# Kernel optimization log

Measured on AMD Instinct MI355X. Metric: run time of the kernel, lower is better.

Reference implementation:

```python
import jax, jax.numpy as jnp
import numpy as np

N, E = 50000, 800000
IN_F, HID, OUT, HEADS = 128, 64, 128, 4
NEG_SLOPE = 0.2


def setup_inputs() -> dict:
    key = jax.random.key(0)
    ks = jax.random.split(key, 10)
    s = 0.05
    return {
        "x": jax.random.normal(ks[0], (N, IN_F), dtype=jnp.float32),
        "edge_index": jax.random.randint(ks[1], (2, E), 0, N, dtype=jnp.int64),
        "W1": jax.random.normal(ks[2], (IN_F, HEADS * HID), dtype=jnp.float32) * s,
        "att_src1": jax.random.normal(ks[3], (HEADS, HID), dtype=jnp.float32) * s,
        "att_dst1": jax.random.normal(ks[4], (HEADS, HID), dtype=jnp.float32) * s,
        "b1": jnp.zeros((HEADS * HID,), dtype=jnp.float32),
        "W2": jax.random.normal(ks[5], (HEADS * HID, OUT), dtype=jnp.float32) * s,
        "att_src2": jax.random.normal(ks[6], (1, OUT), dtype=jnp.float32) * s,
        "att_dst2": jax.random.normal(ks[7], (1, OUT), dtype=jnp.float32) * s,
        "b2": jnp.zeros((OUT,), dtype=jnp.float32),
    }


def _gat_layer(x, W, a_src, a_dst, b, src, dst, heads, out_c):
    n = x.shape[0]
    h = (x @ W).reshape(n, heads, out_c)              # [N, H, C]
    alpha_s = jnp.einsum("nhc,hc->nh", h, a_src)       # [N, H]
    alpha_d = jnp.einsum("nhc,hc->nh", h, a_dst)
    e = jax.nn.leaky_relu(alpha_s[src] + alpha_d[dst], NEG_SLOPE)  # [E, H]
    # scatter-softmax over edges grouped by destination node
    m = jax.ops.segment_max(e, dst, num_segments=n)
    ex = jnp.exp(e - m[dst])
    denom = jax.ops.segment_sum(ex, dst, num_segments=n)
    alpha = ex / denom[dst]                            # [E, H]
    out = jax.ops.segment_sum(alpha[:, :, None] * h[src], dst, num_segments=n)
    return out.reshape(n, heads * out_c) + b


def reference(x, edge_index, W1, att_src1, att_dst1, b1, W2, att_src2, att_dst2, b2):
    n = x.shape[0]
    loop = jnp.arange(n, dtype=edge_index.dtype)       # PyG add_self_loops=True
    src = jnp.concatenate([edge_index[0], loop])
    dst = jnp.concatenate([edge_index[1], loop])
    h = _gat_layer(x, W1, att_src1, att_dst1, b1, src, dst, HEADS, HID)
    h = jax.nn.elu(h)
    out = _gat_layer(h, W2, att_src2, att_dst2, b2, src, dst, 1, OUT)
    return out
```

## Files before the change

kernel.cpp:

```cpp
#include <hip/hip_runtime.h>
#include <hip/hip_bf16.h>

#define NEG_SLOPE 0.2f

typedef short bf16x8 __attribute__((ext_vector_type(8)));
typedef float f32x4 __attribute__((ext_vector_type(4)));
typedef float f32x2 __attribute__((ext_vector_type(2)));

__device__ __forceinline__ unsigned short f2bf(float f) {
    unsigned int x = __float_as_uint(f);
    unsigned int lsb = (x >> 16) & 1u;
    x += 0x7fffu + lsb;
    return (unsigned short)(x >> 16);
}
__device__ __forceinline__ f32x2 upk(unsigned int u) {
    f32x2 r;
    r.x = __uint_as_float(u << 16);
    r.y = __uint_as_float(u & 0xffff0000u);
    return r;
}
__device__ __forceinline__ unsigned short f2h(float f) {
    _Float16 h = (_Float16)f;
    return *(unsigned short*)&h;
}
__device__ __forceinline__ float h2f(unsigned short u) {
    _Float16 h = *(_Float16*)&u;
    return (float)h;
}

__device__ __forceinline__ int bsum_excl(const int* __restrict__ bsum, int nb, int blk) {
    int lane = threadIdx.x & 63;
    int v = (lane < nb) ? bsum[lane] : 0;
    int x = v;
    #pragma unroll
    for (int off = 1; off < 64; off <<= 1) {
        int t = __shfl_up(x, off);
        if (lane >= off) x += t;
    }
    return __shfl(x - v, blk);
}

__global__ void prep_kernel(const float* __restrict__ W1, const float* __restrict__ W2,
                            unsigned short* __restrict__ wt1, unsigned short* __restrict__ wt2,
                            int* __restrict__ deg, int N) {
    int idx = blockIdx.x * 256 + threadIdx.x;
    if (idx < 128 * 256) {
        int k = idx >> 8, n = idx & 255;
        wt1[(size_t)n * 128 + k] = f2bf(W1[idx]);
    } else if (idx < 2 * 128 * 256) {
        int j = idx - 128 * 256;
        int k = j >> 7, n = j & 127;
        wt2[(size_t)n * 256 + k] = f2bf(W2[j]);
    } else {
        int i = idx - 2 * 128 * 256;
        if (i < N) deg[i] = 0;
    }
}

__global__ void degree_kernel(const int* __restrict__ ei, int E, int N,
                              int* __restrict__ deg, int* __restrict__ idx) {
    int e = blockIdx.x * blockDim.x + threadIdx.x;
    int EA = E + N;
    if (e >= EA) return;
    int dst = (e < E) ? ei[E + e] : (e - E);
    idx[e] = atomicAdd(&deg[dst], 1);
}

__global__ void scan_local(const int* __restrict__ deg, int* __restrict__ offs,
                           int* __restrict__ bsum, int N) {
    __shared__ int wsum[16];
    int tid = threadIdx.x;
    int lane = tid & 63;
    int wave = tid >> 6;
    int i = blockIdx.x * 1024 + tid;
    int v = (i < N) ? deg[i] : 0;
    int x = v;
    #pragma unroll
    for (int off = 1; off < 64; off <<= 1) {
        int t = __shfl_up(x, off);
        if (lane >= off) x += t;
    }
    if (lane == 63) wsum[wave] = x;
    __syncthreads();
    if (wave == 0 && lane < 16) {
        int w = wsum[lane];
        #pragma unroll
        for (int off = 1; off < 16; off <<= 1) {
            int t = __shfl_up(w, off);
            if (lane >= off) w += t;
        }
        wsum[lane] = w;
    }
    __syncthreads();
    int wexcl = (wave > 0) ? wsum[wave - 1] : 0;
    if (i <= N) offs[i] = wexcl + x - v;
    if (tid == 0) bsum[blockIdx.x] = wsum[15];
}

__global__ void scatter_kernel(const int* __restrict__ ei, int E, int N,
                               const int* __restrict__ offs, const int* __restrict__ idx,
                               const int* __restrict__ bsum, int nb,
                               const float* __restrict__ as1, const float* __restrict__ ad1,
                               int* __restrict__ colb, uint2* __restrict__ p1) {
    int e = blockIdx.x * blockDim.x + threadIdx.x;
    int EA = E + N;
    bool act = e < EA;
    int s = 0, d = 0;
    if (act) {
        if (e < E) { s = ei[e]; d = ei[E + e]; }
        else       { s = d = e - E; }
    }
    int excl = bsum_excl(bsum, nb, d >> 10);
    if (!act) return;
    int pos = offs[d] + excl + idx[e];
    colb[pos] = s << 9;
    float4 av = *(const float4*)(as1 + s * 4);
    float4 dv = *(const float4*)(ad1 + d * 4);
    float e0 = av.x + dv.x, e1 = av.y + dv.y, e2 = av.z + dv.z, e3 = av.w + dv.w;
    e0 = (e0 > 0.f) ? e0 : NEG_SLOPE * e0;
    e1 = (e1 > 0.f) ? e1 : NEG_SLOPE * e1;
    e2 = (e2 > 0.f) ? e2 : NEG_SLOPE * e2;
    e3 = (e3 > 0.f) ? e3 : NEG_SLOPE * e3;
    uint2 q;
    q.x = (unsigned int)f2h(__expf(e0)) | ((unsigned int)f2h(__expf(e1)) << 16);
    q.y = (unsigned int)f2h(__expf(e2)) | ((unsigned int)f2h(__expf(e3)) << 16);
    p1[pos] = q;
}

__global__ void gemm1_mfma(const float* __restrict__ A,
                           const unsigned short* __restrict__ Wt,
                           const float* __restrict__ att_s, const float* __restrict__ att_d,
                           unsigned short* __restrict__ hb,
                           float* __restrict__ as, float* __restrict__ ad, int M) {
    int wave = threadIdx.x >> 6;
    int lane = threadIdx.x & 63;
    int quad = lane >> 4;
    int l16 = lane & 15;
    int m0 = blockIdx.x * 64 + wave * 16;
    int rowc = min(m0 + l16, M - 1);
    bf16x8 a[4];
    const float* ap = A + (size_t)rowc * 128 + quad * 8;
    #pragma unroll
    for (int kc = 0; kc < 4; ++kc) {
        float4 f0 = *(const float4*)(ap + kc * 32);
        float4 f1 = *(const float4*)(ap + kc * 32 + 4);
        bf16x8 v;
        v[0] = (short)f2bf(f0.x); v[1] = (short)f2bf(f0.y);
        v[2] = (short)f2bf(f0.z); v[3] = (short)f2bf(f0.w);
        v[4] = (short)f2bf(f1.x); v[5] = (short)f2bf(f1.y);
        v[6] = (short)f2bf(f1.z); v[7] = (short)f2bf(f1.w);
        a[kc] = v;
    }
    f32x4 acc[16];
    #pragma unroll
    for (int nt = 0; nt < 16; ++nt) {
        f32x4 c = {0.f, 0.f, 0.f, 0.f};
        const unsigned short* bp = Wt + (size_t)(nt * 16 + l16) * 128 + quad * 8;
        #pragma unroll
        for (int kc = 0; kc < 4; ++kc) {
            bf16x8 b = *(const bf16x8*)(bp + kc * 32);
            c = __builtin_amdgcn_mfma_f32_16x16x32_bf16(a[kc], b, c, 0, 0, 0);
        }
        acc[nt] = c;
    }
    float asv[16], adv[16];
    #pragma unroll
    for (int nt = 0; nt < 16; ++nt) {
        asv[nt] = att_s[nt * 16 + l16];
        adv[nt] = att_d[nt * 16 + l16];
    }
    int srow0 = m0 + quad * 4;
    #pragma unroll
    for (int r = 0; r < 4; ++r) {
        int srow = srow0 + r;
        bool ok = srow < M;
        if (ok) {
            #pragma unroll
            for (int nt = 0; nt < 16; ++nt)
                hb[(size_t)srow * 256 + nt * 16 + l16] = f2bf(acc[nt][r]);
        }
        #pragma unroll
        for (int h = 0; h < 4; ++h) {
            float ps = acc[4 * h][r] * asv[4 * h] + acc[4 * h + 1][r] * asv[4 * h + 1]
                     + acc[4 * h + 2][r] * asv[4 * h + 2] + acc[4 * h + 3][r] * asv[4 * h + 3];
            float pd = acc[4 * h][r] * adv[4 * h] + acc[4 * h + 1][r] * adv[4 * h + 1]
                     + acc[4 * h + 2][r] * adv[4 * h + 2] + acc[4 * h + 3][r] * adv[4 * h + 3];
            #pragma unroll
            for (int off = 1; off < 16; off <<= 1) {
                ps += __shfl_xor(ps, off);
                pd += __shfl_xor(pd, off);
            }
            if (ok && l16 == 0) {
                as[srow * 4 + h] = ps;
                ad[srow * 4 + h] = pd;
            }
        }
    }
}

__global__ void gemm2_mfma(const unsigned short* __restrict__ Ab,
                           const unsigned short* __restrict__ Wt,
                           const float* __restrict__ att_s, const float* __restrict__ att_d,
                           unsigned short* __restrict__ hb,
                           float* __restrict__ as, float* __restrict__ ad, int M) {
    int wave = threadIdx.x >> 6;
    int lane = threadIdx.x & 63;
    int quad = lane >> 4;
    int l16 = lane & 15;
    int m0 = blockIdx.x * 64 + wave * 16;
    int rowc = min(m0 + l16, M - 1);
    bf16x8 a[8];
    const unsigned short* ap = Ab + (size_t)rowc * 256 + quad * 8;
    #pragma unroll
    for (int kc = 0; kc < 8; ++kc) a[kc] = *(const bf16x8*)(ap + kc * 32);
    f32x4 acc[8];
    #pragma unroll
    for (int nt = 0; nt < 8; ++nt) {
        f32x4 c = {0.f, 0.f, 0.f, 0.f};
        const unsigned short* bp = Wt + (size_t)(nt * 16 + l16) * 256 + quad * 8;
        #pragma unroll
        for (int kc = 0; kc < 8; ++kc) {
            bf16x8 b = *(const bf16x8*)(bp + kc * 32);
            c = __builtin_amdgcn_mfma_f32_16x16x32_bf16(a[kc], b, c, 0, 0, 0);
        }
        acc[nt] = c;
    }
    float asv[8], adv[8];
    #pragma unroll
    for (int nt = 0; nt < 8; ++nt) {
        asv[nt] = att_s[nt * 16 + l16];
        adv[nt] = att_d[nt * 16 + l16];
    }
    int srow0 = m0 + quad * 4;
    #pragma unroll
    for (int r = 0; r < 4; ++r) {
        int srow = srow0 + r;
        bool ok = srow < M;
        if (ok) {
            #pragma unroll
            for (int nt = 0; nt < 8; ++nt)
                hb[(size_t)srow * 128 + nt * 16 + l16] = f2bf(acc[nt][r]);
        }
        float ps = 0.f, pd = 0.f;
        #pragma unroll
        for (int nt = 0; nt < 8; ++nt) {
            ps = fmaf(acc[nt][r], asv[nt], ps);
            pd = fmaf(acc[nt][r], adv[nt], pd);
        }
        #pragma unroll
        for (int off = 1; off < 16; off <<= 1) {
            ps += __shfl_xor(ps, off);
            pd += __shfl_xor(pd, off);
        }
        if (ok && l16 == 0) { as[srow] = ps; ad[srow] = pd; }
    }
}

__global__ void agg1_kernel(const unsigned short* __restrict__ hb,
                            const int* __restrict__ colb, const uint2* __restrict__ p1,
                            const int* __restrict__ offs,
                            const int* __restrict__ bsum, int nb,
                            const float* __restrict__ b1,
                            unsigned short* __restrict__ out, int N) {
    int node = blockIdx.x * 4 + (threadIdx.x >> 6);
    if (node >= N) return;
    int lane = threadIdx.x & 63;
    int half = lane >> 5;
    int sub  = lane & 31;
    int head = sub >> 3;
    int c0b = sub * 16;
    const char* hpc = (const char*)hb;
    int beg = offs[node] + bsum_excl(bsum, nb, node >> 10);
    int end = offs[node + 1] + bsum_excl(bsum, nb, (node + 1) >> 10);
    float d = 0.f;
    f32x2 acc[4] = {};
    int j = beg + half;
    for (; j + 6 < end; j += 8) {
        int o0 = colb[j] + c0b;
        int o1 = colb[j + 2] + c0b;
        int o2 = colb[j + 4] + c0b;
        int o3 = colb[j + 6] + c0b;
        uint2 q0 = p1[j];
        uint2 q1 = p1[j + 2];
        uint2 q2 = p1[j + 4];
        uint2 q3 = p1[j + 6];
        uint4 g0 = *(const uint4*)(hpc + o0);
        uint4 g1 = *(const uint4*)(hpc + o1);
        uint4 g2 = *(const uint4*)(hpc + o2);
        uint4 g3 = *(const uint4*)(hpc + o3);
        unsigned int u0 = (head & 2) ? q0.y : q0.x;
        unsigned int u1 = (head & 2) ? q1.y : q1.x;
        unsigned int u2 = (head & 2) ? q2.y : q2.x;
        unsigned int u3 = (head & 2) ? q3.y : q3.x;
        float p0 = h2f((unsigned short)((head & 1) ? (u0 >> 16) : (u0 & 0xffff)));
        float p1v = h2f((unsigned short)((head & 1) ? (u1 >> 16) : (u1 & 0xffff)));
        float p2 = h2f((unsigned short)((head & 1) ? (u2 >> 16) : (u2 & 0xffff)));
        float p3 = h2f((unsigned short)((head & 1) ? (u3 >> 16) : (u3 & 0xffff)));
        d += (p0 + p1v) + (p2 + p3);
        const unsigned int* w0 = (const unsigned int*)&g0;
        const unsigned int* w1 = (const unsigned int*)&g1;
        const unsigned int* w2 = (const unsigned int*)&g2;
        const unsigned int* w3 = (const unsigned int*)&g3;
        f32x2 v0 = {p0, p0}, v1 = {p1v, p1v}, v2 = {p2, p2}, v3 = {p3, p3};
        #pragma unroll
        for (int i = 0; i < 4; ++i) {
            acc[i] = __builtin_elementwise_fma(v0, upk(w0[i]), acc[i]);
            acc[i] = __builtin_elementwise_fma(v1, upk(w1[i]), acc[i]);
            acc[i] = __builtin_elementwise_fma(v2, upk(w2[i]), acc[i]);
            acc[i] = __builtin_elementwise_fma(v3, upk(w3[i]), acc[i]);
        }
    }
    for (; j < end; j += 2) {
        int o = colb[j] + c0b;
        uint2 q = p1[j];
        uint4 g = *(const uint4*)(hpc + o);
        unsigned int u = (head & 2) ? q.y : q.x;
        float p = h2f((unsigned short)((head & 1) ? (u >> 16) : (u & 0xffff)));
        d += p;
        const unsigned int* w = (const unsigned int*)&g;
        f32x2 v = {p, p};
        #pragma unroll
        for (int i = 0; i < 4; ++i)
            acc[i] = __builtin_elementwise_fma(v, upk(w[i]), acc[i]);
    }
    d += __shfl_xor(d, 32);
    #pragma unroll
    for (int i = 0; i < 4; ++i) {
        acc[i].x += __shfl_xor(acc[i].x, 32);
        acc[i].y += __shfl_xor(acc[i].y, 32);
    }
    if (half == 0) {
        float inv = 1.f / d;
        int c0 = sub * 8;
        float4 bb0 = *(const float4*)(b1 + c0);
        float4 bb1 = *(const float4*)(b1 + c0 + 4);
        float av[8] = {acc[0].x, acc[0].y, acc[1].x, acc[1].y,
                       acc[2].x, acc[2].y, acc[3].x, acc[3].y};
        float bb[8] = {bb0.x, bb0.y, bb0.z, bb0.w, bb1.x, bb1.y, bb1.z, bb1.w};
        unsigned short o[8];
        #pragma unroll
        for (int i = 0; i < 8; ++i) {
            float v = av[i] * inv + bb[i];
            v = (v > 0.f) ? v : (__expf(v) - 1.f);
            o[i] = f2bf(v);
        }
        ushort4 q0 = {o[0], o[1], o[2], o[3]};
        ushort4 q1 = {o[4], o[5], o[6], o[7]};
        *(ushort4*)(out + (size_t)node * 256 + c0) = q0;
        *(ushort4*)(out + (size_t)node * 256 + c0 + 4) = q1;
    }
}

__global__ void agg2_kernel(const unsigned short* __restrict__ hb,
                            const float* __restrict__ as,
                            const float* __restrict__ ad,
                            const int* __restrict__ offs, const int* __restrict__ colb,
                            const int* __restrict__ bsum, int nb,
                            const float* __restrict__ b2,
                            float* __restrict__ out, int N) {
    int node = blockIdx.x * 4 + (threadIdx.x >> 6);
    if (node >= N) return;
    int lane = threadIdx.x & 63;
    int q   = lane >> 4;
    int sub = lane & 15;
    int c0b = sub * 16;
    const char* hpc = (const char*)hb;
    float adv = ad[node];
    int beg = offs[node] + bsum_excl(bsum, nb, node >> 10);
    int end = offs[node + 1] + bsum_excl(bsum, nb, (node + 1) >> 10);
    float d = 0.f;
    f32x2 acc[4] = {};
    int j = beg + q;
    for (; j + 4 < end; j += 8) {
        int cb0 = colb[j];
        int cb1 = colb[j + 4];
        uint4 g0 = *(const uint4*)(hpc + (cb0 >> 1) + c0b);
        uint4 g1 = *(const uint4*)(hpc + (cb1 >> 1) + c0b);
        float e0 = as[cb0 >> 9] + adv;
        float e1 = as[cb1 >> 9] + adv;
        e0 = (e0 > 0.f) ? e0 : NEG_SLOPE * e0;
        e1 = (e1 > 0.f) ? e1 : NEG_SLOPE * e1;
        float p0 = __expf(e0), p1 = __expf(e1);
        d += p0 + p1;
        const unsigned int* w0 = (const unsigned int*)&g0;
        const unsigned int* w1 = (const unsigned int*)&g1;
        f32x2 v0 = {p0, p0}, v1 = {p1, p1};
        #pragma unroll
        for (int i = 0; i < 4; ++i) {
            acc[i] = __builtin_elementwise_fma(v0, upk(w0[i]), acc[i]);
            acc[i] = __builtin_elementwise_fma(v1, upk(w1[i]), acc[i]);
        }
    }
    for (; j < end; j += 4) {
        int cb = colb[j];
        uint4 g = *(const uint4*)(hpc + (cb >> 1) + c0b);
        float e = as[cb >> 9] + adv;
        e = (e > 0.f) ? e : NEG_SLOPE * e;
        float p = __expf(e);
        d += p;
        const unsigned int* w = (const unsigned int*)&g;
        f32x2 v = {p, p};
        #pragma unroll
        for (int i = 0; i < 4; ++i)
            acc[i] = __builtin_elementwise_fma(v, upk(w[i]), acc[i]);
    }
    d += __shfl_xor(d, 16);
    d += __shfl_xor(d, 32);
    #pragma unroll
    for (int i = 0; i < 4; ++i) {
        acc[i].x += __shfl_xor(acc[i].x, 16);
        acc[i].x += __shfl_xor(acc[i].x, 32);
        acc[i].y += __shfl_xor(acc[i].y, 16);
        acc[i].y += __shfl_xor(acc[i].y, 32);
    }
    if (lane < 16) {
        float inv = 1.f / d;
        int c0 = sub * 8;
        float4 bb0 = *(const float4*)(b2 + c0);
        float4 bb1 = *(const float4*)(b2 + c0 + 4);
        float av[8] = {acc[0].x, acc[0].y, acc[1].x, acc[1].y,
                       acc[2].x, acc[2].y, acc[3].x, acc[3].y};
        float bb[8] = {bb0.x, bb0.y, bb0.z, bb0.w, bb1.x, bb1.y, bb1.z, bb1.w};
        *(float4*)(out + (size_t)node * 128 + c0) =
            make_float4(av[0] * inv + bb[0], av[1] * inv + bb[1],
                        av[2] * inv + bb[2], av[3] * inv + bb[3]);
        *(float4*)(out + (size_t)node * 128 + c0 + 4) =
            make_float4(av[4] * inv + bb[4], av[5] * inv + bb[5],
                        av[6] * inv + bb[6], av[7] * inv + bb[7]);
    }
}


extern "C" void kernel_launch(void* const* d_in, const int* in_sizes, int n_in,
                              void* d_out, int out_size, void* d_ws, size_t ws_size,
                              hipStream_t stream) {
    const float* x    = (const float*)d_in[0];
    const int*   ei   = (const int*)d_in[1];
    const float* W1   = (const float*)d_in[2];
    const float* at_s1 = (const float*)d_in[3];
    const float* at_d1 = (const float*)d_in[4];
    const float* b1   = (const float*)d_in[5];
    const float* W2   = (const float*)d_in[6];
    const float* at_s2 = (const float*)d_in[7];
    const float* at_d2 = (const float*)d_in[8];
    const float* b2   = (const float*)d_in[9];
    float* out = (float*)d_out;

    const int N  = in_sizes[0] / 128;
    const int E  = in_sizes[1] / 2;
    const int EA = E + N;

    char* ws = (char*)d_ws;
    size_t off = 0;
    auto alloc = [&](size_t bytes) -> void* {
        void* p = ws + off;
        off += (bytes + 255) & ~(size_t)255;
        return p;
    };
    unsigned short* wt1  = (unsigned short*)alloc((size_t)256 * 128 * 2);
    unsigned short* wt2  = (unsigned short*)alloc((size_t)128 * 256 * 2);
    unsigned short* h1b  = (unsigned short*)alloc((size_t)N * 256 * 2);
    unsigned short* h1ab = (unsigned short*)alloc((size_t)N * 256 * 2);
    unsigned short* h2b  = (unsigned short*)alloc((size_t)N * 128 * 2);
    float* as1 = (float*)alloc((size_t)N * 4 * 4);
    float* ad1 = (float*)alloc((size_t)N * 4 * 4);
    float* as2 = (float*)alloc((size_t)N * 4);
    float* ad2 = (float*)alloc((size_t)N * 4);
    int* deg  = (int*)alloc((size_t)N * 4);
    int* idx  = (int*)alloc((size_t)EA * 4);
    int* offs = (int*)alloc((size_t)(N + 1) * 4);
    int* bsum = (int*)alloc((size_t)1024 * 4);
    int* colb = (int*)alloc((size_t)EA * 4);
    uint2* p1 = (uint2*)alloc((size_t)EA * 8);

    const int nb = (N + 1 + 1023) / 1024;

    prep_kernel<<<(2 * 128 * 256 + N + 255) / 256, 256, 0, stream>>>(W1, W2, wt1, wt2, deg, N);
    degree_kernel<<<(EA + 255) / 256, 256, 0, stream>>>(ei, E, N, deg, idx);
    scan_local<<<nb, 1024, 0, stream>>>(deg, offs, bsum, N);

    gemm1_mfma<<<(N + 63) / 64, 256, 0, stream>>>(x, wt1, at_s1, at_d1, h1b, as1, ad1, N);
    scatter_kernel<<<(EA + 255) / 256, 256, 0, stream>>>(ei, E, N, offs, idx, bsum, nb,
                                                         as1, ad1, colb, p1);
    agg1_kernel<<<(N + 3) / 4, 256, 0, stream>>>(h1b, colb, p1, offs, bsum, nb, b1, h1ab, N);

    gemm2_mfma<<<(N + 63) / 64, 256, 0, stream>>>(h1ab, wt2, at_s2, at_d2, h2b, as2, ad2, N);
    agg2_kernel<<<(N + 3) / 4, 256, 0, stream>>>(h2b, as2, ad2, offs, colb, bsum, nb,
                                                 b2, out, N);
}
```

Measured before the change: 332.9 us.

## Fuse layer-1 aggregation with layer-2 GEMM through shared-memory tile

Merges agg1 and gemm2 into one kernel. Each block aggregates 16 nodes (4 per wave) into an LDS bf16 tile, then runs MFMA against W2, with each wave covering 2 of the 8 output column tiles and combining the attention dot products via LDS atomics. This removes the global write and re-read of the N×256 intermediate and one kernel launch. In exchange each wave now processes 4 nodes one after another, the block has a barrier before the GEMM, and every block reloads W2 from cache.

```diff
diff --git a/kernel.cpp b/kernel.cpp
--- a/kernel.cpp
+++ b/kernel.cpp
@@ -198,156 +198,158 @@
     }
 }
 
-__global__ void gemm2_mfma(const unsigned short* __restrict__ Ab,
+__global__ void agg1_gemm2(const unsigned short* __restrict__ hb,
+                           const int* __restrict__ colb, const uint2* __restrict__ p1,
+                           const int* __restrict__ offs,
+                           const int* __restrict__ bsum, int nb,
+                           const float* __restrict__ b1,
                            const unsigned short* __restrict__ Wt,
                            const float* __restrict__ att_s, const float* __restrict__ att_d,
-                           unsigned short* __restrict__ hb,
-                           float* __restrict__ as, float* __restrict__ ad, int M) {
-    int wave = threadIdx.x >> 6;
-    int lane = threadIdx.x & 63;
-    int quad = lane >> 4;
-    int l16 = lane & 15;
-    int m0 = blockIdx.x * 64 + wave * 16;
-    int rowc = min(m0 + l16, M - 1);
-    bf16x8 a[8];
-    const unsigned short* ap = Ab + (size_t)rowc * 256 + quad * 8;
-    #pragma unroll
-    for (int kc = 0; kc < 8; ++kc) a[kc] = *(const bf16x8*)(ap + kc * 32);
-    f32x4 acc[8];
-    #pragma unroll
-    for (int nt = 0; nt < 8; ++nt) {
-        f32x4 c = {0.f, 0.f, 0.f, 0.f};
-        const unsigned short* bp = Wt + (size_t)(nt * 16 + l16) * 256 + quad * 8;
-        #pragma unroll
-        for (int kc = 0; kc < 8; ++kc) {
-            bf16x8 b = *(const bf16x8*)(bp + kc * 32);
-            c = __builtin_amdgcn_mfma_f32_16x16x32_bf16(a[kc], b, c, 0, 0, 0);
-        }
-        acc[nt] = c;
-    }
-    float asv[8], adv[8];
-    #pragma unroll
-    for (int nt = 0; nt < 8; ++nt) {
-        asv[nt] = att_s[nt * 16 + l16];
-        adv[nt] = att_d[nt * 16 + l16];
-    }
-    int srow0 = m0 + quad * 4;
-    #pragma unroll
-    for (int r = 0; r < 4; ++r) {
-        int srow = srow0 + r;
-        bool ok = srow < M;
-        if (ok) {
-            #pragma unroll
-            for (int nt = 0; nt < 8; ++nt)
-                hb[(size_t)srow * 128 + nt * 16 + l16] = f2bf(acc[nt][r]);
-        }
-        float ps = 0.f, pd = 0.f;
-        #pragma unroll
-        for (int nt = 0; nt < 8; ++nt) {
-            ps = fmaf(acc[nt][r], asv[nt], ps);
-            pd = fmaf(acc[nt][r], adv[nt], pd);
-        }
-        #pragma unroll
-        for (int off = 1; off < 16; off <<= 1) {
-            ps += __shfl_xor(ps, off);
-            pd += __shfl_xor(pd, off);
-        }
-        if (ok && l16 == 0) { as[srow] = ps; ad[srow] = pd; }
-    }
-}
-
-__global__ void agg1_kernel(const unsigned short* __restrict__ hb,
-                            const int* __restrict__ colb, const uint2* __restrict__ p1,
-                            const int* __restrict__ offs,
-                            const int* __restrict__ bsum, int nb,
-                            const float* __restrict__ b1,
-                            unsigned short* __restrict__ out, int N) {
-    int node = blockIdx.x * 4 + (threadIdx.x >> 6);
-    if (node >= N) return;
-    int lane = threadIdx.x & 63;
+                           unsigned short* __restrict__ h2b,
+                           float* __restrict__ as2, float* __restrict__ ad2, int N) {
+    __shared__ unsigned short Atile[16][264];
+    __shared__ float asP[16], adP[16];
+    int tid = threadIdx.x;
+    int wave = tid >> 6;
+    int lane = tid & 63;
+    if (tid < 16) { asP[tid] = 0.f; adP[tid] = 0.f; }
     int half = lane >> 5;
     int sub  = lane & 31;
     int head = sub >> 3;
     int c0b = sub * 16;
     const char* hpc = (const char*)hb;
-    int beg = offs[node] + bsum_excl(bsum, nb, node >> 10);
-    int end = offs[node + 1] + bsum_excl(bsum, nb, (node + 1) >> 10);
-    float d = 0.f;
-    f32x2 acc[4] = {};
-    int j = beg + half;
-    for (; j + 6 < end; j += 8) {
-        int o0 = colb[j] + c0b;
-        int o1 = colb[j + 2] + c0b;
-        int o2 = colb[j + 4] + c0b;
-        int o3 = colb[j + 6] + c0b;
-        uint2 q0 = p1[j];
-        uint2 q1 = p1[j + 2];
-        uint2 q2 = p1[j + 4];
-        uint2 q3 = p1[j + 6];
-        uint4 g0 = *(const uint4*)(hpc + o0);
-        uint4 g1 = *(const uint4*)(hpc + o1);
-        uint4 g2 = *(const uint4*)(hpc + o2);
-        uint4 g3 = *(const uint4*)(hpc + o3);
-        unsigned int u0 = (head & 2) ? q0.y : q0.x;
-        unsigned int u1 = (head & 2) ? q1.y : q1.x;
-        unsigned int u2 = (head & 2) ? q2.y : q2.x;
-        unsigned int u3 = (head & 2) ? q3.y : q3.x;
-        float p0 = h2f((unsigned short)((head & 1) ? (u0 >> 16) : (u0 & 0xffff)));
-        float p1v = h2f((unsigned short)((head & 1) ? (u1 >> 16) : (u1 & 0xffff)));
-        float p2 = h2f((unsigned short)((head & 1) ? (u2 >> 16) : (u2 & 0xffff)));
-        float p3 = h2f((unsigned short)((head & 1) ? (u3 >> 16) : (u3 & 0xffff)));
-        d += (p0 + p1v) + (p2 + p3);
-        const unsigned int* w0 = (const unsigned int*)&g0;
-        const unsigned int* w1 = (const unsigned int*)&g1;
-        const unsigned int* w2 = (const unsigned int*)&g2;
-        const unsigned int* w3 = (const unsigned int*)&g3;
-        f32x2 v0 = {p0, p0}, v1 = {p1v, p1v}, v2 = {p2, p2}, v3 = {p3, p3};
+    int node0 = blockIdx.x * 16;
+
+    for (int t = 0; t < 4; ++t) {
+        int lrow = wave * 4 + t;
+        int node = min(node0 + lrow, N - 1);
+        int beg = offs[node] + bsum_excl(bsum, nb, node >> 10);
+        int end = offs[node + 1] + bsum_excl(bsum, nb, (node + 1) >> 10);
+        float d = 0.f;
+        f32x2 acc[4] = {};
+        int j = beg + half;
+        for (; j + 6 < end; j += 8) {
+            int o0 = colb[j] + c0b;
+            int o1 = colb[j + 2] + c0b;
+            int o2 = colb[j + 4] + c0b;
+            int o3 = colb[j + 6] + c0b;
+            uint2 q0 = p1[j];
+            uint2 q1 = p1[j + 2];
+            uint2 q2 = p1[j + 4];
+            uint2 q3 = p1[j + 6];
+            uint4 g0 = *(const uint4*)(hpc + o0);
+            uint4 g1 = *(const uint4*)(hpc + o1);
+            uint4 g2 = *(const uint4*)(hpc + o2);
+            uint4 g3 = *(const uint4*)(hpc + o3);
+            unsigned int u0 = (head & 2) ? q0.y : q0.x;
+            unsigned int u1 = (head & 2) ? q1.y : q1.x;
+            unsigned int u2 = (head & 2) ? q2.y : q2.x;
+            unsigned int u3 = (head & 2) ? q3.y : q3.x;
+            float p0 = h2f((unsigned short)((head & 1) ? (u0 >> 16) : (u0 & 0xffff)));
+            float p1v = h2f((unsigned short)((head & 1) ? (u1 >> 16) : (u1 & 0xffff)));
+            float p2 = h2f((unsigned short)((head & 1) ? (u2 >> 16) : (u2 & 0xffff)));
+            float p3 = h2f((unsigned short)((head & 1) ? (u3 >> 16) : (u3 & 0xffff)));
+            d += (p0 + p1v) + (p2 + p3);
+            const unsigned int* w0 = (const unsigned int*)&g0;
+            const unsigned int* w1 = (const unsigned int*)&g1;
+            const unsigned int* w2 = (const unsigned int*)&g2;
+            const unsigned int* w3 = (const unsigned int*)&g3;
+            f32x2 v0 = {p0, p0}, v1 = {p1v, p1v}, v2 = {p2, p2}, v3 = {p3, p3};
+            #pragma unroll
+            for (int i = 0; i < 4; ++i) {
+                acc[i] = __builtin_elementwise_fma(v0, upk(w0[i]), acc[i]);
+                acc[i] = __builtin_elementwise_fma(v1, upk(w1[i]), acc[i]);
+                acc[i] = __builtin_elementwise_fma(v2, upk(w2[i]), acc[i]);
+                acc[i] = __builtin_elementwise_fma(v3, upk(w3[i]), acc[i]);
+            }
+        }
+        for (; j < end; j += 2) {
+            int o = colb[j] + c0b;
+            uint2 q = p1[j];
+            uint4 g = *(const uint4*)(hpc + o);
+            unsigned int u = (head & 2) ? q.y : q.x;
+            float p = h2f((unsigned short)((head & 1) ? (u >> 16) : (u & 0xffff)));
+            d += p;
+            const unsigned int* w = (const unsigned int*)&g;
+            f32x2 v = {p, p};
+            #pragma unroll
+            for (int i = 0; i < 4; ++i)
+                acc[i] = __builtin_elementwise_fma(v, upk(w[i]), acc[i]);
+        }
+        d += __shfl_xor(d, 32);
         #pragma unroll
         for (int i = 0; i < 4; ++i) {
-            acc[i] = __builtin_elementwise_fma(v0, upk(w0[i]), acc[i]);
-            acc[i] = __builtin_elementwise_fma(v1, upk(w1[i]), acc[i]);
-            acc[i] = __builtin_elementwise_fma(v2, upk(w2[i]), acc[i]);
-            acc[i] = __builtin_elementwise_fma(v3, upk(w3[i]), acc[i]);
-        }
-    }
-    for (; j < end; j += 2) {
-        int o = colb[j] + c0b;
-        uint2 q = p1[j];
-        uint4 g = *(const uint4*)(hpc + o);
-        unsigned int u = (head & 2) ? q.y : q.x;
-        float p = h2f((unsigned short)((head & 1) ? (u >> 16) : (u & 0xffff)));
-        d += p;
-        const unsigned int* w = (const unsigned int*)&g;
-        f32x2 v = {p, p};
-        #pragma unroll
-        for (int i = 0; i < 4; ++i)
-            acc[i] = __builtin_elementwise_fma(v, upk(w[i]), acc[i]);
-    }
-    d += __shfl_xor(d, 32);
-    #pragma unroll
-    for (int i = 0; i < 4; ++i) {
-        acc[i].x += __shfl_xor(acc[i].x, 32);
-        acc[i].y += __shfl_xor(acc[i].y, 32);
-    }
-    if (half == 0) {
-        float inv = 1.f / d;
-        int c0 = sub * 8;
-        float4 bb0 = *(const float4*)(b1 + c0);
-        float4 bb1 = *(const float4*)(b1 + c0 + 4);
-        float av[8] = {acc[0].x, acc[0].y, acc[1].x, acc[1].y,
-                       acc[2].x, acc[2].y, acc[3].x, acc[3].y};
-        float bb[8] = {bb0.x, bb0.y, bb0.z, bb0.w, bb1.x, bb1.y, bb1.z, bb1.w};
-        unsigned short o[8];
-        #pragma unroll
-        for (int i = 0; i < 8; ++i) {
-            float v = av[i] * inv + bb[i];
-            v = (v > 0.f) ? v : (__expf(v) - 1.f);
-            o[i] = f2bf(v);
-        }
-        ushort4 q0 = {o[0], o[1], o[2], o[3]};
-        ushort4 q1 = {o[4], o[5], o[6], o[7]};
-        *(ushort4*)(out + (size_t)node * 256 + c0) = q0;
-        *(ushort4*)(out + (size_t)node * 256 + c0 + 4) = q1;
+            acc[i].x += __shfl_xor(acc[i].x, 32);
+            acc[i].y += __shfl_xor(acc[i].y, 32);
+        }
+        if (half == 0) {
+            float inv = 1.f / d;
+            int c0 = sub * 8;
+            float4 bb0 = *(const float4*)(b1 + c0);
+            float4 bb1 = *(const float4*)(b1 + c0 + 4);
+            float av[8] = {acc[0].x, acc[0].y, acc[1].x, acc[1].y,
+                           acc[2].x, acc[2].y, acc[3].x, acc[3].y};
+            float bb[8] = {bb0.x, bb0.y, bb0.z, bb0.w, bb1.x, bb1.y, bb1.z, bb1.w};
+            unsigned short o[8];
+            #pragma unroll
+            for (int i = 0; i < 8; ++i) {
+                float v = av[i] * inv + bb[i];
+                v = (v > 0.f) ? v : (__expf(v) - 1.f);
+                o[i] = f2bf(v);
+            }
+            ushort4 q0 = {o[0], o[1], o[2], o[3]};
+            ushort4 q1 = {o[4], o[5], o[6], o[7]};
+            *(ushort4*)&Atile[lrow][c0] = q0;
+            *(ushort4*)&Atile[lrow][c0 + 4] = q1;
+        }
+    }
+    __syncthreads();
+
+    int quad = lane >> 4;
+    int l16 = lane & 15;
+    bf16x8 a[8];
+    #pragma unroll
+    for (int kc = 0; kc < 8; ++kc)
+        a[kc] = *(const bf16x8*)&Atile[l16][kc * 32 + quad * 8];
+    int nt0 = wave * 2;
+    f32x4 acc2[2];
+    #pragma unroll
+    for (int i = 0; i < 2; ++i) {
+        f32x4 c = {0.f, 0.f, 0.f, 0.f};
+        const unsigned short* bp = Wt + (size_t)((nt0 + i) * 16 + l16) * 256 + quad * 8;
+        #pragma unroll
+        for (int kc = 0; kc < 8; ++kc) {
+            bf16x8 b = *(const bf16x8*)(bp + kc * 32);
+            c = __builtin_amdgcn_mfma_f32_16x16x32_bf16(a[kc], b, c, 0, 0, 0);
+        }
+        acc2[i] = c;
+    }
+    float s0 = att_s[nt0 * 16 + l16], s1 = att_s[(nt0 + 1) * 16 + l16];
+    float d0 = att_d[nt0 * 16 + l16], d1 = att_d[(nt0 + 1) * 16 + l16];
+    #pragma unroll
+    for (int r = 0; r < 4; ++r) {
+        int row = quad * 4 + r;
+        int grow = node0 + row;
+        if (grow < N) {
+            h2b[(size_t)grow * 128 + nt0 * 16 + l16] = f2bf(acc2[0][r]);
+            h2b[(size_t)grow * 128 + (nt0 + 1) * 16 + l16] = f2bf(acc2[1][r]);
+        }
+        float ps = acc2[0][r] * s0 + acc2[1][r] * s1;
+        float pd = acc2[0][r] * d0 + acc2[1][r] * d1;
+        #pragma unroll
+        for (int off = 1; off < 16; off <<= 1) {
+            ps += __shfl_xor(ps, off);
+            pd += __shfl_xor(pd, off);
+        }
+        if (l16 == 0) {
+            atomicAdd(&asP[row], ps);
+            atomicAdd(&adP[row], pd);
+        }
+    }
+    __syncthreads();
+    if (tid < 16 && node0 + tid < N) {
+        as2[node0 + tid] = asP[tid];
+        ad2[node0 + tid] = adP[tid];
     }
 }
 
@@ -460,7 +462,6 @@
     unsigned short* wt1  = (unsigned short*)alloc((size_t)256 * 128 * 2);
     unsigned short* wt2  = (unsigned short*)alloc((size_t)128 * 256 * 2);
     unsigned short* h1b  = (unsigned short*)alloc((size_t)N * 256 * 2);
-    unsigned short* h1ab = (unsigned short*)alloc((size_t)N * 256 * 2);
     unsigned short* h2b  = (unsigned short*)alloc((size_t)N * 128 * 2);
     float* as1 = (float*)alloc((size_t)N * 4 * 4);
     float* ad1 = (float*)alloc((size_t)N * 4 * 4);
@@ -482,9 +483,8 @@
     gemm1_mfma<<<(N + 63) / 64, 256, 0, stream>>>(x, wt1, at_s1, at_d1, h1b, as1, ad1, N);
     scatter_kernel<<<(EA + 255) / 256, 256, 0, stream>>>(ei, E, N, offs, idx, bsum, nb,
                                                          as1, ad1, colb, p1);
-    agg1_kernel<<<(N + 3) / 4, 256, 0, stream>>>(h1b, colb, p1, offs, bsum, nb, b1, h1ab, N);
-
-    gemm2_mfma<<<(N + 63) / 64, 256, 0, stream>>>(h1ab, wt2, at_s2, at_d2, h2b, as2, ad2, N);
+    agg1_gemm2<<<(N + 15) / 16, 256, 0, stream>>>(h1b, colb, p1, offs, bsum, nb, b1,
+                                                  wt2, at_s2, at_d2, h2b, as2, ad2, N);
     agg2_kernel<<<(N + 3) / 4, 256, 0, stream>>>(h2b, as2, ad2, offs, colb, bsum, nb,
                                                  b2, out, N);
 }
```

Measured after the change: 325.8 us. 2.1% less time.

## Fuse layer-1 aggregation with layer-2 GEMM through an LDS tile

Applied to the files above, without the earlier changes.

Merges the agg1 kernel and gemm2 kernel into one. Each wave aggregates 16 nodes one after another and writes the ELU-activated bf16 rows into an XOR-swizzled shared-memory tile, which then feeds the MFMA GEMM directly. This removes the global write and re-read of the 50000x256 intermediate and one kernel launch. In exchange, each wave handles 16 nodes serially with only 4 waves per block, which lowers the parallelism of the gather phase and may hurt latency hiding. The edge loop may also be unbalanced across the 16 nodes.

```diff
diff --git a/kernel.cpp b/kernel.cpp
--- a/kernel.cpp
+++ b/kernel.cpp
@@ -198,156 +198,160 @@
     }
 }
 
-__global__ void gemm2_mfma(const unsigned short* __restrict__ Ab,
+__global__ void agg1_gemm2(const unsigned short* __restrict__ hb,
+                           const int* __restrict__ colb, const uint2* __restrict__ p1,
+                           const int* __restrict__ offs,
+                           const int* __restrict__ bsum, int nb,
+                           const float* __restrict__ b1,
                            const unsigned short* __restrict__ Wt,
                            const float* __restrict__ att_s, const float* __restrict__ att_d,
-                           unsigned short* __restrict__ hb,
-                           float* __restrict__ as, float* __restrict__ ad, int M) {
-    int wave = threadIdx.x >> 6;
-    int lane = threadIdx.x & 63;
-    int quad = lane >> 4;
-    int l16 = lane & 15;
-    int m0 = blockIdx.x * 64 + wave * 16;
-    int rowc = min(m0 + l16, M - 1);
-    bf16x8 a[8];
-    const unsigned short* ap = Ab + (size_t)rowc * 256 + quad * 8;
-    #pragma unroll
-    for (int kc = 0; kc < 8; ++kc) a[kc] = *(const bf16x8*)(ap + kc * 32);
-    f32x4 acc[8];
-    #pragma unroll
-    for (int nt = 0; nt < 8; ++nt) {
-        f32x4 c = {0.f, 0.f, 0.f, 0.f};
-        const unsigned short* bp = Wt + (size_t)(nt * 16 + l16) * 256 + quad * 8;
-        #pragma unroll
-        for (int kc = 0; kc < 8; ++kc) {
-            bf16x8 b = *(const bf16x8*)(bp + kc * 32);
-            c = __builtin_amdgcn_mfma_f32_16x16x32_bf16(a[kc], b, c, 0, 0, 0);
-        }
-        acc[nt] = c;
-    }
-    float asv[8], adv[8];
-    #pragma unroll
-    for (int nt = 0; nt < 8; ++nt) {
-        asv[nt] = att_s[nt * 16 + l16];
-        adv[nt] = att_d[nt * 16 + l16];
-    }
-    int srow0 = m0 + quad * 4;
-    #pragma unroll
-    for (int r = 0; r < 4; ++r) {
-        int srow = srow0 + r;
-        bool ok = srow < M;
-        if (ok) {
-            #pragma unroll
-            for (int nt = 0; nt < 8; ++nt)
-                hb[(size_t)srow * 128 + nt * 16 + l16] = f2bf(acc[nt][r]);
-        }
-        float ps = 0.f, pd = 0.f;
-        #pragma unroll
-        for (int nt = 0; nt < 8; ++nt) {
-            ps = fmaf(acc[nt][r], asv[nt], ps);
-            pd = fmaf(acc[nt][r], adv[nt], pd);
-        }
-        #pragma unroll
-        for (int off = 1; off < 16; off <<= 1) {
-            ps += __shfl_xor(ps, off);
-            pd += __shfl_xor(pd, off);
-        }
-        if (ok && l16 == 0) { as[srow] = ps; ad[srow] = pd; }
-    }
-}
-
-__global__ void agg1_kernel(const unsigned short* __restrict__ hb,
-                            const int* __restrict__ colb, const uint2* __restrict__ p1,
-                            const int* __restrict__ offs,
-                            const int* __restrict__ bsum, int nb,
-                            const float* __restrict__ b1,
-                            unsigned short* __restrict__ out, int N) {
-    int node = blockIdx.x * 4 + (threadIdx.x >> 6);
-    if (node >= N) return;
-    int lane = threadIdx.x & 63;
+                           unsigned short* __restrict__ h2b,
+                           float* __restrict__ as2, float* __restrict__ ad2, int N) {
+    __shared__ unsigned short tiles[4][16][256];
+    int tid = threadIdx.x;
+    int wave = tid >> 6;
+    int lane = tid & 63;
     int half = lane >> 5;
     int sub  = lane & 31;
     int head = sub >> 3;
     int c0b = sub * 16;
     const char* hpc = (const char*)hb;
-    int beg = offs[node] + bsum_excl(bsum, nb, node >> 10);
-    int end = offs[node + 1] + bsum_excl(bsum, nb, (node + 1) >> 10);
-    float d = 0.f;
-    f32x2 acc[4] = {};
-    int j = beg + half;
-    for (; j + 6 < end; j += 8) {
-        int o0 = colb[j] + c0b;
-        int o1 = colb[j + 2] + c0b;
-        int o2 = colb[j + 4] + c0b;
-        int o3 = colb[j + 6] + c0b;
-        uint2 q0 = p1[j];
-        uint2 q1 = p1[j + 2];
-        uint2 q2 = p1[j + 4];
-        uint2 q3 = p1[j + 6];
-        uint4 g0 = *(const uint4*)(hpc + o0);
-        uint4 g1 = *(const uint4*)(hpc + o1);
-        uint4 g2 = *(const uint4*)(hpc + o2);
-        uint4 g3 = *(const uint4*)(hpc + o3);
-        unsigned int u0 = (head & 2) ? q0.y : q0.x;
-        unsigned int u1 = (head & 2) ? q1.y : q1.x;
-        unsigned int u2 = (head & 2) ? q2.y : q2.x;
-        unsigned int u3 = (head & 2) ? q3.y : q3.x;
-        float p0 = h2f((unsigned short)((head & 1) ? (u0 >> 16) : (u0 & 0xffff)));
-        float p1v = h2f((unsigned short)((head & 1) ? (u1 >> 16) : (u1 & 0xffff)));
-        float p2 = h2f((unsigned short)((head & 1) ? (u2 >> 16) : (u2 & 0xffff)));
-        float p3 = h2f((unsigned short)((head & 1) ? (u3 >> 16) : (u3 & 0xffff)));
-        d += (p0 + p1v) + (p2 + p3);
-        const unsigned int* w0 = (const unsigned int*)&g0;
-        const unsigned int* w1 = (const unsigned int*)&g1;
-        const unsigned int* w2 = (const unsigned int*)&g2;
-        const unsigned int* w3 = (const unsigned int*)&g3;
-        f32x2 v0 = {p0, p0}, v1 = {p1v, p1v}, v2 = {p2, p2}, v3 = {p3, p3};
+    int node0 = blockIdx.x * 64 + wave * 16;
+    unsigned short (*tile)[256] = tiles[wave];
+
+    for (int t = 0; t < 16; ++t) {
+        int node = min(node0 + t, N - 1);
+        int beg = offs[node] + bsum_excl(bsum, nb, node >> 10);
+        int end = offs[node + 1] + bsum_excl(bsum, nb, (node + 1) >> 10);
+        float d = 0.f;
+        f32x2 acc[4] = {};
+        int j = beg + half;
+        for (; j + 6 < end; j += 8) {
+            int o0 = colb[j] + c0b;
+            int o1 = colb[j + 2] + c0b;
+            int o2 = colb[j + 4] + c0b;
+            int o3 = colb[j + 6] + c0b;
+            uint2 q0 = p1[j];
+            uint2 q1 = p1[j + 2];
+            uint2 q2 = p1[j + 4];
+            uint2 q3 = p1[j + 6];
+            uint4 g0 = *(const uint4*)(hpc + o0);
+            uint4 g1 = *(const uint4*)(hpc + o1);
+            uint4 g2 = *(const uint4*)(hpc + o2);
+            uint4 g3 = *(const uint4*)(hpc + o3);
+            unsigned int u0 = (head & 2) ? q0.y : q0.x;
+            unsigned int u1 = (head & 2) ? q1.y : q1.x;
+            unsigned int u2 = (head & 2) ? q2.y : q2.x;
+            unsigned int u3 = (head & 2) ? q3.y : q3.x;
+            float p0 = h2f((unsigned short)((head & 1) ? (u0 >> 16) : (u0 & 0xffff)));
+            float p1v = h2f((unsigned short)((head & 1) ? (u1 >> 16) : (u1 & 0xffff)));
+            float p2 = h2f((unsigned short)((head & 1) ? (u2 >> 16) : (u2 & 0xffff)));
+            float p3 = h2f((unsigned short)((head & 1) ? (u3 >> 16) : (u3 & 0xffff)));
+            d += (p0 + p1v) + (p2 + p3);
+            const unsigned int* w0 = (const unsigned int*)&g0;
+            const unsigned int* w1 = (const unsigned int*)&g1;
+            const unsigned int* w2 = (const unsigned int*)&g2;
+            const unsigned int* w3 = (const unsigned int*)&g3;
+            f32x2 v0 = {p0, p0}, v1 = {p1v, p1v}, v2 = {p2, p2}, v3 = {p3, p3};
+            #pragma unroll
+            for (int i = 0; i < 4; ++i) {
+                acc[i] = __builtin_elementwise_fma(v0, upk(w0[i]), acc[i]);
+                acc[i] = __builtin_elementwise_fma(v1, upk(w1[i]), acc[i]);
+                acc[i] = __builtin_elementwise_fma(v2, upk(w2[i]), acc[i]);
+                acc[i] = __builtin_elementwise_fma(v3, upk(w3[i]), acc[i]);
+            }
+        }
+        for (; j < end; j += 2) {
+            int o = colb[j] + c0b;
+            uint2 q = p1[j];
+            uint4 g = *(const uint4*)(hpc + o);
+            unsigned int u = (head & 2) ? q.y : q.x;
+            float p = h2f((unsigned short)((head & 1) ? (u >> 16) : (u & 0xffff)));
+            d += p;
+            const unsigned int* w = (const unsigned int*)&g;
+            f32x2 v = {p, p};
+            #pragma unroll
+            for (int i = 0; i < 4; ++i)
+                acc[i] = __builtin_elementwise_fma(v, upk(w[i]), acc[i]);
+        }
+        d += __shfl_xor(d, 32);
         #pragma unroll
         for (int i = 0; i < 4; ++i) {
-            acc[i] = __builtin_elementwise_fma(v0, upk(w0[i]), acc[i]);
-            acc[i] = __builtin_elementwise_fma(v1, upk(w1[i]), acc[i]);
-            acc[i] = __builtin_elementwise_fma(v2, upk(w2[i]), acc[i]);
-            acc[i] = __builtin_elementwise_fma(v3, upk(w3[i]), acc[i]);
-        }
-    }
-    for (; j < end; j += 2) {
-        int o = colb[j] + c0b;
-        uint2 q = p1[j];
-        uint4 g = *(const uint4*)(hpc + o);
-        unsigned int u = (head & 2) ? q.y : q.x;
-        float p = h2f((unsigned short)((head & 1) ? (u >> 16) : (u & 0xffff)));
-        d += p;
-        const unsigned int* w = (const unsigned int*)&g;
-        f32x2 v = {p, p};
-        #pragma unroll
-        for (int i = 0; i < 4; ++i)
-            acc[i] = __builtin_elementwise_fma(v, upk(w[i]), acc[i]);
-    }
-    d += __shfl_xor(d, 32);
-    #pragma unroll
-    for (int i = 0; i < 4; ++i) {
-        acc[i].x += __shfl_xor(acc[i].x, 32);
-        acc[i].y += __shfl_xor(acc[i].y, 32);
-    }
-    if (half == 0) {
-        float inv = 1.f / d;
-        int c0 = sub * 8;
-        float4 bb0 = *(const float4*)(b1 + c0);
-        float4 bb1 = *(const float4*)(b1 + c0 + 4);
-        float av[8] = {acc[0].x, acc[0].y, acc[1].x, acc[1].y,
-                       acc[2].x, acc[2].y, acc[3].x, acc[3].y};
-        float bb[8] = {bb0.x, bb0.y, bb0.z, bb0.w, bb1.x, bb1.y, bb1.z, bb1.w};
-        unsigned short o[8];
-        #pragma unroll
-        for (int i = 0; i < 8; ++i) {
-            float v = av[i] * inv + bb[i];
-            v = (v > 0.f) ? v : (__expf(v) - 1.f);
-            o[i] = f2bf(v);
-        }
-        ushort4 q0 = {o[0], o[1], o[2], o[3]};
-        ushort4 q1 = {o[4], o[5], o[6], o[7]};
-        *(ushort4*)(out + (size_t)node * 256 + c0) = q0;
-        *(ushort4*)(out + (size_t)node * 256 + c0 + 4) = q1;
+            acc[i].x += __shfl_xor(acc[i].x, 32);
+            acc[i].y += __shfl_xor(acc[i].y, 32);
+        }
+        if (half == 0) {
+            float inv = 1.f / d;
+            int c0 = sub * 8;
+            float4 bb0 = *(const float4*)(b1 + c0);
+            float4 bb1 = *(const float4*)(b1 + c0 + 4);
+            float av[8] = {acc[0].x, acc[0].y, acc[1].x, acc[1].y,
+                           acc[2].x, acc[2].y, acc[3].x, acc[3].y};
+            float bb[8] = {bb0.x, bb0.y, bb0.z, bb0.w, bb1.x, bb1.y, bb1.z, bb1.w};
+            unsigned short o[8];
+            #pragma unroll
+            for (int i = 0; i < 8; ++i) {
+                float v = av[i] * inv + bb[i];
+                v = (v > 0.f) ? v : (__expf(v) - 1.f);
+                o[i] = f2bf(v);
+            }
+            uint4 pk;
+            pk.x = (unsigned int)o[0] | ((unsigned int)o[1] << 16);
+            pk.y = (unsigned int)o[2] | ((unsigned int)o[3] << 16);
+            pk.z = (unsigned int)o[4] | ((unsigned int)o[5] << 16);
+            pk.w = (unsigned int)o[6] | ((unsigned int)o[7] << 16);
+            *(uint4*)&tile[t][(sub ^ t) * 8] = pk;
+        }
+    }
+
+    int quad = lane >> 4;
+    int l16 = lane & 15;
+    bf16x8 a[8];
+    #pragma unroll
+    for (int kc = 0; kc < 8; ++kc) {
+        int grp = (kc * 4 + quad) ^ l16;
+        a[kc] = *(const bf16x8*)&tile[l16][grp * 8];
+    }
+    f32x4 acc2[8];
+    #pragma unroll
+    for (int nt = 0; nt < 8; ++nt) {
+        f32x4 c = {0.f, 0.f, 0.f, 0.f};
+        const unsigned short* bp = Wt + (size_t)(nt * 16 + l16) * 256 + quad * 8;
+        #pragma unroll
+        for (int kc = 0; kc < 8; ++kc) {
+            bf16x8 b = *(const bf16x8*)(bp + kc * 32);
+            c = __builtin_amdgcn_mfma_f32_16x16x32_bf16(a[kc], b, c, 0, 0, 0);
+        }
+        acc2[nt] = c;
+    }
+    float asv[8], adv[8];
+    #pragma unroll
+    for (int nt = 0; nt < 8; ++nt) {
+        asv[nt] = att_s[nt * 16 + l16];
+        adv[nt] = att_d[nt * 16 + l16];
+    }
+    int srow0 = node0 + quad * 4;
+    #pragma unroll
+    for (int r = 0; r < 4; ++r) {
+        int srow = srow0 + r;
+        bool ok = srow < N;
+        if (ok) {
+            #pragma unroll
+            for (int nt = 0; nt < 8; ++nt)
+                h2b[(size_t)srow * 128 + nt * 16 + l16] = f2bf(acc2[nt][r]);
+        }
+        float ps = 0.f, pd = 0.f;
+        #pragma unroll
+        for (int nt = 0; nt < 8; ++nt) {
+            ps = fmaf(acc2[nt][r], asv[nt], ps);
+            pd = fmaf(acc2[nt][r], adv[nt], pd);
+        }
+        #pragma unroll
+        for (int off = 1; off < 16; off <<= 1) {
+            ps += __shfl_xor(ps, off);
+            pd += __shfl_xor(pd, off);
+        }
+        if (ok && l16 == 0) { as2[srow] = ps; ad2[srow] = pd; }
     }
 }
 
@@ -460,7 +464,6 @@
     unsigned short* wt1  = (unsigned short*)alloc((size_t)256 * 128 * 2);
     unsigned short* wt2  = (unsigned short*)alloc((size_t)128 * 256 * 2);
     unsigned short* h1b  = (unsigned short*)alloc((size_t)N * 256 * 2);
-    unsigned short* h1ab = (unsigned short*)alloc((size_t)N * 256 * 2);
     unsigned short* h2b  = (unsigned short*)alloc((size_t)N * 128 * 2);
     float* as1 = (float*)alloc((size_t)N * 4 * 4);
     float* ad1 = (float*)alloc((size_t)N * 4 * 4);
@@ -482,9 +485,8 @@
     gemm1_mfma<<<(N + 63) / 64, 256, 0, stream>>>(x, wt1, at_s1, at_d1, h1b, as1, ad1, N);
     scatter_kernel<<<(EA + 255) / 256, 256, 0, stream>>>(ei, E, N, offs, idx, bsum, nb,
                                                          as1, ad1, colb, p1);
-    agg1_kernel<<<(N + 3) / 4, 256, 0, stream>>>(h1b, colb, p1, offs, bsum, nb, b1, h1ab, N);
-
-    gemm2_mfma<<<(N + 63) / 64, 256, 0, stream>>>(h1ab, wt2, at_s2, at_d2, h2b, as2, ad2, N);
+    agg1_gemm2<<<(N + 63) / 64, 256, 0, stream>>>(h1b, colb, p1, offs, bsum, nb, b1,
+                                                  wt2, at_s2, at_d2, h2b, as2, ad2, N);
     agg2_kernel<<<(N + 3) / 4, 256, 0, stream>>>(h2b, as2, ad2, offs, colb, bsum, nb,
                                                  b2, out, N);
 }
```

After: 340.5 us. 1.02x slower.
